# Kernel optimization log

Measured on AMD Instinct MI355X. Metric: run time of the kernel, lower is better.

## Reference

```python
import jax, jax.numpy as jnp
import numpy as np

N_NODES = 100000
N_EDGES = 1600000
IN_DIM, HID_DIM, OUT_DIM = 128, 64, 64


def setup_inputs() -> dict:
    key = jax.random.key(0)
    ks = jax.random.split(key, 8)
    x = jax.random.normal(ks[0], (N_NODES, IN_DIM), dtype=jnp.float32)
    edge_index = jax.random.randint(ks[1], (2, N_EDGES), 0, N_NODES, dtype=jnp.int32)
    edge_weight = jax.random.uniform(ks[2], (N_EDGES,), dtype=jnp.float32)
    # GCNConv parameters (glorot-ish init)
    w1 = jax.random.normal(ks[3], (IN_DIM, HID_DIM), dtype=jnp.float32) / np.sqrt(IN_DIM)
    b1 = jnp.zeros((HID_DIM,), dtype=jnp.float32)
    w2 = jax.random.normal(ks[4], (HID_DIM, OUT_DIM), dtype=jnp.float32) / np.sqrt(HID_DIM)
    b2 = jnp.zeros((OUT_DIM,), dtype=jnp.float32)
    return {"x": x, "edge_index": edge_index, "edge_weight": edge_weight,
            "w1": w1, "b1": b1, "w2": w2, "b2": b2}


def _gcn_conv(h, src, dst, edge_weight, w, b, n_nodes):
    # GCNConv(normalize=False): linear transform, then edge-weighted scatter-add
    # (source_to_target flow: gather from src, scatter-sum into dst), then bias.
    h = h @ w                                   # [N, out]
    msg = h[src] * edge_weight[:, None]          # [E, out] irregular gather
    agg = jax.ops.segment_sum(msg, dst, num_segments=n_nodes)  # [N, out]
    return agg + b


def reference(x, edge_index, edge_weight, w1, b1, w2, b2):
    src, dst = edge_index[0], edge_index[1]
    n = x.shape[0]
    # Dropout is identity in eval mode (training=False).
    h = _gcn_conv(x, src, dst, edge_weight, w1, b1, n)
    h = jax.nn.relu(h)
    out = _gcn_conv(h, src, dst, edge_weight, w2, b2, n)
    return out
```

## Files before the change

### kernel.cpp

```cpp
#include <hip/hip_runtime.h>
#include <hip/hip_bf16.h>


#define N_NODES 100000
#define N_EDGES 1600000
#define NB1     196
#define T1      4096
#define NT1     391

typedef unsigned short ushort_t;
typedef unsigned int uint_t;
typedef __attribute__((ext_vector_type(8))) short bf16x8;
typedef __attribute__((ext_vector_type(4))) float floatx4;
typedef __attribute__((ext_vector_type(8))) ushort_t ushort8v;

static __device__ __forceinline__ float bf2f(ushort_t h) {
    return __uint_as_float(((uint_t)h) << 16);
}
static __device__ __forceinline__ ushort_t f2bf(float f) {
    uint_t u = __float_as_uint(f);
    u = (u + 0x7FFF + ((u >> 16) & 1)) >> 16;
    return (ushort_t)u;
}

__global__ __launch_bounds__(512) void k_count1(
    const int* __restrict__ dst, int* __restrict__ counts, int E)
{
    __shared__ int cnt[NB1];
    const int t = threadIdx.x;
    if (t < NB1) cnt[t] = 0;
    __syncthreads();
    const int e0 = blockIdx.x * T1;
    const int e1 = min(E, e0 + T1);
    for (int e = e0 + t; e < e1; e += 512)
        atomicAdd(&cnt[dst[e] >> 9], 1);
    __syncthreads();
    if (t < NB1) counts[(size_t)blockIdx.x * NB1 + t] = cnt[t];
}

__global__ __launch_bounds__(512) void k_cscan(
    const int* __restrict__ counts, int* __restrict__ offs,
    int* __restrict__ ctot)
{
    __shared__ int s[512];
    const int t = threadIdx.x, k = blockIdx.x;
    const int v = (t < NT1) ? counts[(size_t)t * NB1 + k] : 0;
    s[t] = v;
    #pragma unroll
    for (int off = 1; off < 512; off <<= 1) {
        __syncthreads();
        int a = (t >= off) ? s[t - off] : 0;
        __syncthreads();
        s[t] += a;
    }
    __syncthreads();
    if (t < NT1) offs[(size_t)t * NB1 + k] = s[t] - v;
    if (t == 511) ctot[k] = s[511];
}

__global__ __launch_bounds__(256) void k_tscan(
    const int* __restrict__ ctot, int* __restrict__ cbase)
{
    __shared__ int s[256];
    const int t = threadIdx.x;
    const int v = (t < NB1) ? ctot[t] : 0;
    s[t] = v;
    #pragma unroll
    for (int off = 1; off < 256; off <<= 1) {
        __syncthreads();
        int a = (t >= off) ? s[t - off] : 0;
        __syncthreads();
        s[t] += a;
    }
    __syncthreads();
    if (t < NB1) cbase[t] = s[t] - v;
}

__global__ __launch_bounds__(512) void k_pass1(
    const int* __restrict__ src, const int* __restrict__ dst,
    const float* __restrict__ ew, const int* __restrict__ offs,
    const int* __restrict__ cbase, int2* __restrict__ recs1, int E)
{
    __shared__ int cnt[NB1], start[NB1], cursor[NB1], gb[NB1];
    __shared__ int s[256];
    __shared__ int2 stg[T1];
    __shared__ unsigned char sb[T1];
    const int t = threadIdx.x, b = blockIdx.x;

    if (t < NB1) cnt[t] = 0;
    __syncthreads();
    const int e0 = b * T1;
    const int e1 = min(E, e0 + T1);
    for (int e = e0 + t; e < e1; e += 512)
        atomicAdd(&cnt[dst[e] >> 9], 1);
    __syncthreads();
    int v = 0;
    if (t < 256) { v = (t < NB1) ? cnt[t] : 0; s[t] = v; }
    #pragma unroll
    for (int off = 1; off < 256; off <<= 1) {
        __syncthreads();
        int a = (t < 256 && t >= off) ? s[t - off] : 0;
        __syncthreads();
        if (t < 256) s[t] += a;
    }
    __syncthreads();
    if (t < NB1) {
        int st = s[t] - v;
        start[t]  = st;
        cursor[t] = st;
        gb[t]     = cbase[t] + offs[(size_t)b * NB1 + t];
    }
    __syncthreads();
    for (int e = e0 + t; e < e1; e += 512) {
        int d  = dst[e];
        int bk = d >> 9;
        int p  = atomicAdd(&cursor[bk], 1);
        int2 r;
        r.x = ((d & 511) << 17) | src[e];
        r.y = __float_as_int(ew[e]);
        stg[p] = r;
        sb[p]  = (unsigned char)bk;
    }
    __syncthreads();
    const int n = e1 - e0;
    for (int i = t; i < n; i += 512) {
        int bk = sb[i];
        recs1[gb[bk] + (i - start[bk])] = stg[i];
    }
}

__global__ __launch_bounds__(512) void k_pass2(
    const int2* __restrict__ recs1, const int* __restrict__ cbase,
    const int* __restrict__ ctot, int2* __restrict__ recs2,
    int* __restrict__ node_start, int* __restrict__ node_cnt, int N)
{
    __shared__ int cnt[512];
    __shared__ int s[512];
    __shared__ int cursor[512];
    const int t = threadIdx.x, b = blockIdx.x;
    const int lo = cbase[b];
    const int hi = lo + ctot[b];

    cnt[t] = 0;
    __syncthreads();
    for (int j = lo + t; j < hi; j += 512)
        atomicAdd(&cnt[((uint_t)recs1[j].x) >> 17], 1);
    __syncthreads();
    const int v = cnt[t];
    s[t] = v;
    #pragma unroll
    for (int off = 1; off < 512; off <<= 1) {
        __syncthreads();
        int a = (t >= off) ? s[t - off] : 0;
        __syncthreads();
        s[t] += a;
    }
    __syncthreads();
    const int stl = s[t] - v;
    cursor[t] = stl;
    const int ng = b * 512 + t;
    if (ng < N) {
        node_start[ng] = lo + stl;
        node_cnt[ng]   = v;
    }
    __syncthreads();
    for (int j = lo + t; j < hi; j += 512) {
        int2 r = recs1[j];
        int dl = ((uint_t)r.x) >> 17;
        int p  = atomicAdd(&cursor[dl], 1);
        int2 o;
        o.x = r.x & 0x1FFFF;
        o.y = r.y;
        recs2[lo + p] = o;
    }
}

__global__ __launch_bounds__(256) void k_gemm1(
    const float* __restrict__ X, const float* __restrict__ W,
    ushort_t* __restrict__ Y, int N)
{
    __shared__ ushort_t sA[64 * 136];
    __shared__ ushort_t sB[64 * 136];
    const int tid  = threadIdx.x;
    const int row0 = blockIdx.x * 64;

    for (int i = tid; i < 64 * 32; i += 256) {
        int r = i >> 5, c4 = (i & 31) * 4;
        int rg = row0 + r; if (rg > N - 1) rg = N - 1;
        float4 v = *(const float4*)(X + (size_t)rg * 128 + c4);
        ushort4 pk = make_ushort4(f2bf(v.x), f2bf(v.y), f2bf(v.z), f2bf(v.w));
        *(ushort4*)(sA + r * 136 + c4) = pk;
    }
    for (int i = tid; i < 128 * 16; i += 256) {
        int k = i >> 4, n4 = (i & 15) * 4;
        float4 v = *(const float4*)(W + (size_t)k * 64 + n4);
        sB[(n4 + 0) * 136 + k] = f2bf(v.x);
        sB[(n4 + 1) * 136 + k] = f2bf(v.y);
        sB[(n4 + 2) * 136 + k] = f2bf(v.z);
        sB[(n4 + 3) * 136 + k] = f2bf(v.w);
    }
    __syncthreads();

    const int wid = tid >> 6, lane = tid & 63;
    const int m = lane & 15, quad = lane >> 4;
    floatx4 acc[4] = {};

    #pragma unroll
    for (int ks = 0; ks < 4; ++ks) {
        bf16x8 a = *(const bf16x8*)(sA + (wid * 16 + m) * 136 + ks * 32 + quad * 8);
        #pragma unroll
        for (int nt = 0; nt < 4; ++nt) {
            bf16x8 bfr = *(const bf16x8*)(sB + (nt * 16 + m) * 136 + ks * 32 + quad * 8);
            acc[nt] = __builtin_amdgcn_mfma_f32_16x16x32_bf16(a, bfr, acc[nt], 0, 0, 0);
        }
    }
    #pragma unroll
    for (int nt = 0; nt < 4; ++nt)
        #pragma unroll
        for (int r = 0; r < 4; ++r) {
            int grow = row0 + wid * 16 + quad * 4 + r;
            if (grow < N)
                Y[(size_t)grow * 64 + nt * 16 + m] = f2bf(acc[nt][r]);
        }
}

__global__ __launch_bounds__(256) void k_gemm2(
    const ushort_t* __restrict__ X, const float* __restrict__ W,
    ushort_t* __restrict__ Y, int N)
{
    __shared__ ushort_t sA[64 * 72];
    __shared__ ushort_t sB[64 * 72];
    const int tid  = threadIdx.x;
    const int row0 = blockIdx.x * 64;

    for (int i = tid; i < 64 * 16; i += 256) {
        int r = i >> 4, c4 = (i & 15) * 4;
        int rg = row0 + r; if (rg > N - 1) rg = N - 1;
        *(ushort4*)(sA + r * 72 + c4) =
            *(const ushort4*)(X + (size_t)rg * 64 + c4);
    }
    for (int i = tid; i < 64 * 16; i += 256) {
        int k = i >> 4, n4 = (i & 15) * 4;
        float4 v = *(const float4*)(W + (size_t)k * 64 + n4);
        sB[(n4 + 0) * 72 + k] = f2bf(v.x);
        sB[(n4 + 1) * 72 + k] = f2bf(v.y);
        sB[(n4 + 2) * 72 + k] = f2bf(v.z);
        sB[(n4 + 3) * 72 + k] = f2bf(v.w);
    }
    __syncthreads();

    const int wid = tid >> 6, lane = tid & 63;
    const int m = lane & 15, quad = lane >> 4;
    floatx4 acc[4] = {};

    #pragma unroll
    for (int ks = 0; ks < 2; ++ks) {
        bf16x8 a = *(const bf16x8*)(sA + (wid * 16 + m) * 72 + ks * 32 + quad * 8);
        #pragma unroll
        for (int nt = 0; nt < 4; ++nt) {
            bf16x8 bfr = *(const bf16x8*)(sB + (nt * 16 + m) * 72 + ks * 32 + quad * 8);
            acc[nt] = __builtin_amdgcn_mfma_f32_16x16x32_bf16(a, bfr, acc[nt], 0, 0, 0);
        }
    }
    #pragma unroll
    for (int nt = 0; nt < 4; ++nt)
        #pragma unroll
        for (int r = 0; r < 4; ++r) {
            int grow = row0 + wid * 16 + quad * 4 + r;
            if (grow < N)
                Y[(size_t)grow * 64 + nt * 16 + m] = f2bf(acc[nt][r]);
        }
}

template<bool RELU, bool OUT_BF16>
__global__ __launch_bounds__(256) void k_gather(
    const ushort_t* __restrict__ H, const int2* __restrict__ recs,
    const int* __restrict__ node_start, const int* __restrict__ node_cnt,
    const float* __restrict__ bias, void* __restrict__ out)
{
    const int wid  = threadIdx.x >> 6;
    const int lane = threadIdx.x & 63;
    const int n    = blockIdx.x * 4 + wid;

    const int start = node_start[n];
    const int end   = start + node_cnt[n];
    const int oct   = lane >> 3;
    const int c8    = (lane & 7) * 8;

    float a[8];
    #pragma unroll
    for (int i = 0; i < 8; ++i) a[i] = 0.f;

    for (int base = start; base < end; base += 64) {
        const int m = (end - base < 64) ? (end - base) : 64;
        int2 r = recs[base + (lane < m ? lane : 0)];
        float rw = __int_as_float(r.y);
        #pragma unroll 8
        for (int jj = 0; jj < m; jj += 8) {
            int idx = jj + oct;
            int s   = __shfl(r.x, idx);
            float w = __shfl(rw, idx);
            if (idx >= m) w = 0.f;
            ushort8v hv = *(const ushort8v*)(H + (size_t)s * 64 + c8);
            #pragma unroll
            for (int i = 0; i < 8; ++i)
                a[i] = fmaf(w, bf2f(hv[i]), a[i]);
        }
    }
    #pragma unroll
    for (int i = 0; i < 8; ++i) {
        a[i] += __shfl_down(a[i], 32);
        a[i] += __shfl_down(a[i], 16);
        a[i] += __shfl_down(a[i], 8);
    }

    if (lane < 8) {
        float4 b0 = *(const float4*)(bias + c8);
        float4 b1v = *(const float4*)(bias + c8 + 4);
        float v[8];
        v[0] = a[0] + b0.x;  v[1] = a[1] + b0.y;
        v[2] = a[2] + b0.z;  v[3] = a[3] + b0.w;
        v[4] = a[4] + b1v.x; v[5] = a[5] + b1v.y;
        v[6] = a[6] + b1v.z; v[7] = a[7] + b1v.w;
        if (RELU) {
            #pragma unroll
            for (int i = 0; i < 8; ++i) v[i] = fmaxf(v[i], 0.f);
        }
        if (OUT_BF16) {
            ushort8v pk;
            #pragma unroll
            for (int i = 0; i < 8; ++i) pk[i] = f2bf(v[i]);
            *(ushort8v*)((ushort_t*)out + (size_t)n * 64 + c8) = pk;
        } else {
            *(float4*)((float*)out + (size_t)n * 64 + c8) =
                make_float4(v[0], v[1], v[2], v[3]);
            *(float4*)((float*)out + (size_t)n * 64 + c8 + 4) =
                make_float4(v[4], v[5], v[6], v[7]);
        }
    }
}

extern "C" void kernel_launch(void* const* d_in, const int* in_sizes, int n_in,
                              void* d_out, int out_size, void* d_ws, size_t ws_size,
                              hipStream_t stream) {
    const float* x   = (const float*)d_in[0];
    const int*   ei  = (const int*)  d_in[1];
    const float* ew  = (const float*)d_in[2];
    const float* w1  = (const float*)d_in[3];
    const float* b1  = (const float*)d_in[4];
    const float* w2  = (const float*)d_in[5];
    const float* b2  = (const float*)d_in[6];
    float* out = (float*)d_out;

    const int N = N_NODES, E = N_EDGES;
    const int* src = ei;
    const int* dst = ei + E;

    char* p = (char*)d_ws;
    ushort_t* bufA   = (ushort_t*)p;  p += (size_t)N_NODES * 64 * 2;
    int2*     recs2  = (int2*)p;      p += (size_t)N_EDGES * 8;
    int2*     recs1  = (int2*)p;
    ushort_t* bufB   = (ushort_t*)p;  p += (size_t)N_EDGES * 8;
    int*      counts = (int*)p;       p += (size_t)NT1 * NB1 * 4;
    int*      offs   = (int*)p;       p += (size_t)NT1 * NB1 * 4;
    int*      ctot   = (int*)p;       p += 1024;
    int*      cbase  = (int*)p;       p += 1024;
    int*      nstart = (int*)p;       p += (size_t)N_NODES * 4;
    int*      ncnt   = (int*)p;       p += (size_t)N_NODES * 4;

    k_count1<<<NT1, 512, 0, stream>>>(dst, counts, E);
    k_cscan <<<NB1, 512, 0, stream>>>(counts, offs, ctot);
    k_tscan <<<1,   256, 0, stream>>>(ctot, cbase);
    k_pass1 <<<NT1, 512, 0, stream>>>(src, dst, ew, offs, cbase, recs1, E);
    k_pass2 <<<NB1, 512, 0, stream>>>(recs1, cbase, ctot, recs2, nstart, ncnt, N);

    k_gemm1<<<(N + 63) / 64, 256, 0, stream>>>(x, w1, bufA, N);
    k_gather<true, true><<<N / 4, 256, 0, stream>>>(bufA, recs2, nstart, ncnt, b1, bufB);

    k_gemm2<<<(N + 63) / 64, 256, 0, stream>>>(bufB, w2, bufA, N);
    k_gather<false, false><<<N / 4, 256, 0, stream>>>(bufA, recs2, nstart, ncnt, b2, out);
}
```

Measured before the change: 262.1 us.

## Use finer dst buckets, pack node info, stage GEMM stores, simplify gather

Doubles the number of coarse destination buckets, going from 512 nodes each to 256, so the second sort pass uses 256-thread blocks and more of them. Node start and count are packed into one int2 array. The GEMM epilogues now stage results in shared memory and write coalesced 16-byte rows. The gather kernel is rewritten so each edge is handled by 16 lanes with 4-wide loads, removing the shuffle-broadcast loop. Together these aim to cut sort overhead and improve memory access patterns, at the cost of narrower per-lane loads in the gather and an extra shared-memory round trip in the GEMMs.

```diff
diff --git a/kernel.cpp b/kernel.cpp
--- a/kernel.cpp
+++ b/kernel.cpp
@@ -4,7 +4,7 @@
 
 #define N_NODES 100000
 #define N_EDGES 1600000
-#define NB1     196
+#define NB1     391
 #define T1      4096
 #define NT1     391
 
@@ -33,7 +33,7 @@
     const int e0 = blockIdx.x * T1;
     const int e1 = min(E, e0 + T1);
     for (int e = e0 + t; e < e1; e += 512)
-        atomicAdd(&cnt[dst[e] >> 9], 1);
+        atomicAdd(&cnt[dst[e] >> 8], 1);
     __syncthreads();
     if (t < NB1) counts[(size_t)blockIdx.x * NB1 + t] = cnt[t];
 }
@@ -58,15 +58,15 @@
     if (t == 511) ctot[k] = s[511];
 }
 
-__global__ __launch_bounds__(256) void k_tscan(
+__global__ __launch_bounds__(512) void k_tscan(
     const int* __restrict__ ctot, int* __restrict__ cbase)
 {
-    __shared__ int s[256];
+    __shared__ int s[512];
     const int t = threadIdx.x;
     const int v = (t < NB1) ? ctot[t] : 0;
     s[t] = v;
     #pragma unroll
-    for (int off = 1; off < 256; off <<= 1) {
+    for (int off = 1; off < 512; off <<= 1) {
         __syncthreads();
         int a = (t >= off) ? s[t - off] : 0;
         __syncthreads();
@@ -82,9 +82,9 @@
     const int* __restrict__ cbase, int2* __restrict__ recs1, int E)
 {
     __shared__ int cnt[NB1], start[NB1], cursor[NB1], gb[NB1];
-    __shared__ int s[256];
+    __shared__ int s[512];
     __shared__ int2 stg[T1];
-    __shared__ unsigned char sb[T1];
+    __shared__ ushort_t sb[T1];
     const int t = threadIdx.x, b = blockIdx.x;
 
     if (t < NB1) cnt[t] = 0;
@@ -92,16 +92,16 @@
     const int e0 = b * T1;
     const int e1 = min(E, e0 + T1);
     for (int e = e0 + t; e < e1; e += 512)
-        atomicAdd(&cnt[dst[e] >> 9], 1);
-    __syncthreads();
-    int v = 0;
-    if (t < 256) { v = (t < NB1) ? cnt[t] : 0; s[t] = v; }
-    #pragma unroll
-    for (int off = 1; off < 256; off <<= 1) {
-        __syncthreads();
-        int a = (t < 256 && t >= off) ? s[t - off] : 0;
-        __syncthreads();
-        if (t < 256) s[t] += a;
+        atomicAdd(&cnt[dst[e] >> 8], 1);
+    __syncthreads();
+    const int v = (t < NB1) ? cnt[t] : 0;
+    s[t] = v;
+    #pragma unroll
+    for (int off = 1; off < 512; off <<= 1) {
+        __syncthreads();
+        int a = (t >= off) ? s[t - off] : 0;
+        __syncthreads();
+        s[t] += a;
     }
     __syncthreads();
     if (t < NB1) {
@@ -113,13 +113,13 @@
     __syncthreads();
     for (int e = e0 + t; e < e1; e += 512) {
         int d  = dst[e];
-        int bk = d >> 9;
+        int bk = d >> 8;
         int p  = atomicAdd(&cursor[bk], 1);
         int2 r;
-        r.x = ((d & 511) << 17) | src[e];
+        r.x = ((d & 255) << 17) | src[e];
         r.y = __float_as_int(ew[e]);
         stg[p] = r;
-        sb[p]  = (unsigned char)bk;
+        sb[p]  = (ushort_t)bk;
     }
     __syncthreads();
     const int n = e1 - e0;
@@ -129,27 +129,27 @@
     }
 }
 
-__global__ __launch_bounds__(512) void k_pass2(
+__global__ __launch_bounds__(256) void k_pass2(
     const int2* __restrict__ recs1, const int* __restrict__ cbase,
     const int* __restrict__ ctot, int2* __restrict__ recs2,
-    int* __restrict__ node_start, int* __restrict__ node_cnt, int N)
-{
-    __shared__ int cnt[512];
-    __shared__ int s[512];
-    __shared__ int cursor[512];
+    int2* __restrict__ nodeinfo, int N)
+{
+    __shared__ int cnt[256];
+    __shared__ int s[256];
+    __shared__ int cursor[256];
     const int t = threadIdx.x, b = blockIdx.x;
     const int lo = cbase[b];
     const int hi = lo + ctot[b];
 
     cnt[t] = 0;
     __syncthreads();
-    for (int j = lo + t; j < hi; j += 512)
+    for (int j = lo + t; j < hi; j += 256)
         atomicAdd(&cnt[((uint_t)recs1[j].x) >> 17], 1);
     __syncthreads();
     const int v = cnt[t];
     s[t] = v;
     #pragma unroll
-    for (int off = 1; off < 512; off <<= 1) {
+    for (int off = 1; off < 256; off <<= 1) {
         __syncthreads();
         int a = (t >= off) ? s[t - off] : 0;
         __syncthreads();
@@ -158,13 +158,13 @@
     __syncthreads();
     const int stl = s[t] - v;
     cursor[t] = stl;
-    const int ng = b * 512 + t;
+    const int ng = b * 256 + t;
     if (ng < N) {
-        node_start[ng] = lo + stl;
-        node_cnt[ng]   = v;
-    }
-    __syncthreads();
-    for (int j = lo + t; j < hi; j += 512) {
+        int2 ni; ni.x = lo + stl; ni.y = v;
+        nodeinfo[ng] = ni;
+    }
+    __syncthreads();
+    for (int j = lo + t; j < hi; j += 256) {
         int2 r = recs1[j];
         int dl = ((uint_t)r.x) >> 17;
         int p  = atomicAdd(&cursor[dl], 1);
@@ -214,14 +214,20 @@
             acc[nt] = __builtin_amdgcn_mfma_f32_16x16x32_bf16(a, bfr, acc[nt], 0, 0, 0);
         }
     }
+    __syncthreads();
     #pragma unroll
     for (int nt = 0; nt < 4; ++nt)
         #pragma unroll
-        for (int r = 0; r < 4; ++r) {
-            int grow = row0 + wid * 16 + quad * 4 + r;
-            if (grow < N)
-                Y[(size_t)grow * 64 + nt * 16 + m] = f2bf(acc[nt][r]);
-        }
+        for (int r = 0; r < 4; ++r)
+            sA[(wid * 16 + quad * 4 + r) * 72 + nt * 16 + m] = f2bf(acc[nt][r]);
+    __syncthreads();
+    for (int i = tid; i < 64 * 8; i += 256) {
+        int rr = i >> 3, c8 = (i & 7) * 8;
+        int rg = row0 + rr;
+        if (rg < N)
+            *(ushort8v*)(Y + (size_t)rg * 64 + c8) =
+                *(const ushort8v*)(sA + rr * 72 + c8);
+    }
 }
 
 __global__ __launch_bounds__(256) void k_gemm2(
@@ -262,80 +268,71 @@
             acc[nt] = __builtin_amdgcn_mfma_f32_16x16x32_bf16(a, bfr, acc[nt], 0, 0, 0);
         }
     }
+    __syncthreads();
     #pragma unroll
     for (int nt = 0; nt < 4; ++nt)
         #pragma unroll
-        for (int r = 0; r < 4; ++r) {
-            int grow = row0 + wid * 16 + quad * 4 + r;
-            if (grow < N)
-                Y[(size_t)grow * 64 + nt * 16 + m] = f2bf(acc[nt][r]);
-        }
+        for (int r = 0; r < 4; ++r)
+            sA[(wid * 16 + quad * 4 + r) * 72 + nt * 16 + m] = f2bf(acc[nt][r]);
+    __syncthreads();
+    for (int i = tid; i < 64 * 8; i += 256) {
+        int rr = i >> 3, c8 = (i & 7) * 8;
+        int rg = row0 + rr;
+        if (rg < N)
+            *(ushort8v*)(Y + (size_t)rg * 64 + c8) =
+                *(const ushort8v*)(sA + rr * 72 + c8);
+    }
 }
 
 template<bool RELU, bool OUT_BF16>
 __global__ __launch_bounds__(256) void k_gather(
     const ushort_t* __restrict__ H, const int2* __restrict__ recs,
-    const int* __restrict__ node_start, const int* __restrict__ node_cnt,
-    const float* __restrict__ bias, void* __restrict__ out)
+    const int2* __restrict__ nodeinfo, const float* __restrict__ bias,
+    void* __restrict__ out)
 {
     const int wid  = threadIdx.x >> 6;
     const int lane = threadIdx.x & 63;
     const int n    = blockIdx.x * 4 + wid;
 
-    const int start = node_start[n];
-    const int end   = start + node_cnt[n];
-    const int oct   = lane >> 3;
-    const int c8    = (lane & 7) * 8;
-
-    float a[8];
-    #pragma unroll
-    for (int i = 0; i < 8; ++i) a[i] = 0.f;
-
-    for (int base = start; base < end; base += 64) {
-        const int m = (end - base < 64) ? (end - base) : 64;
-        int2 r = recs[base + (lane < m ? lane : 0)];
-        float rw = __int_as_float(r.y);
-        #pragma unroll 8
-        for (int jj = 0; jj < m; jj += 8) {
-            int idx = jj + oct;
-            int s   = __shfl(r.x, idx);
-            float w = __shfl(rw, idx);
-            if (idx >= m) w = 0.f;
-            ushort8v hv = *(const ushort8v*)(H + (size_t)s * 64 + c8);
-            #pragma unroll
-            for (int i = 0; i < 8; ++i)
-                a[i] = fmaf(w, bf2f(hv[i]), a[i]);
-        }
-    }
-    #pragma unroll
-    for (int i = 0; i < 8; ++i) {
-        a[i] += __shfl_down(a[i], 32);
-        a[i] += __shfl_down(a[i], 16);
-        a[i] += __shfl_down(a[i], 8);
-    }
-
-    if (lane < 8) {
-        float4 b0 = *(const float4*)(bias + c8);
-        float4 b1v = *(const float4*)(bias + c8 + 4);
-        float v[8];
-        v[0] = a[0] + b0.x;  v[1] = a[1] + b0.y;
-        v[2] = a[2] + b0.z;  v[3] = a[3] + b0.w;
-        v[4] = a[4] + b1v.x; v[5] = a[5] + b1v.y;
-        v[6] = a[6] + b1v.z; v[7] = a[7] + b1v.w;
+    const int2 ni   = nodeinfo[n];
+    const int start = ni.x;
+    const int cnt   = ni.y;
+    const int end   = start + cnt;
+    const int g     = lane >> 4;
+    const int c4    = (lane & 15) * 4;
+    const int trip  = (cnt + 3) >> 2;
+
+    float a0 = 0.f, a1 = 0.f, a2 = 0.f, a3 = 0.f;
+    int j = start + g;
+    #pragma unroll 2
+    for (int k = 0; k < trip; ++k, j += 4) {
+        int jc = (j < end) ? j : (end - 1);
+        int2 r = recs[jc];
+        float w = (j < end) ? __int_as_float(r.y) : 0.f;
+        ushort4 hv = *(const ushort4*)(H + (size_t)r.x * 64 + c4);
+        a0 = fmaf(w, bf2f(hv.x), a0);
+        a1 = fmaf(w, bf2f(hv.y), a1);
+        a2 = fmaf(w, bf2f(hv.z), a2);
+        a3 = fmaf(w, bf2f(hv.w), a3);
+    }
+    a0 += __shfl_down(a0, 32); a1 += __shfl_down(a1, 32);
+    a2 += __shfl_down(a2, 32); a3 += __shfl_down(a3, 32);
+    a0 += __shfl_down(a0, 16); a1 += __shfl_down(a1, 16);
+    a2 += __shfl_down(a2, 16); a3 += __shfl_down(a3, 16);
+
+    if (lane < 16) {
+        float4 bv = *(const float4*)(bias + c4);
+        float v0 = a0 + bv.x, v1 = a1 + bv.y, v2 = a2 + bv.z, v3 = a3 + bv.w;
         if (RELU) {
-            #pragma unroll
-            for (int i = 0; i < 8; ++i) v[i] = fmaxf(v[i], 0.f);
+            v0 = fmaxf(v0, 0.f); v1 = fmaxf(v1, 0.f);
+            v2 = fmaxf(v2, 0.f); v3 = fmaxf(v3, 0.f);
         }
         if (OUT_BF16) {
-            ushort8v pk;
-            #pragma unroll
-            for (int i = 0; i < 8; ++i) pk[i] = f2bf(v[i]);
-            *(ushort8v*)((ushort_t*)out + (size_t)n * 64 + c8) = pk;
+            ushort4 pk = make_ushort4(f2bf(v0), f2bf(v1), f2bf(v2), f2bf(v3));
+            *(ushort4*)((ushort_t*)out + (size_t)n * 64 + c4) = pk;
         } else {
-            *(float4*)((float*)out + (size_t)n * 64 + c8) =
-                make_float4(v[0], v[1], v[2], v[3]);
-            *(float4*)((float*)out + (size_t)n * 64 + c8 + 4) =
-                make_float4(v[4], v[5], v[6], v[7]);
+            *(float4*)((float*)out + (size_t)n * 64 + c4) =
+                make_float4(v0, v1, v2, v3);
         }
     }
 }
@@ -363,20 +360,19 @@
     ushort_t* bufB   = (ushort_t*)p;  p += (size_t)N_EDGES * 8;
     int*      counts = (int*)p;       p += (size_t)NT1 * NB1 * 4;
     int*      offs   = (int*)p;       p += (size_t)NT1 * NB1 * 4;
-    int*      ctot   = (int*)p;       p += 1024;
-    int*      cbase  = (int*)p;       p += 1024;
-    int*      nstart = (int*)p;       p += (size_t)N_NODES * 4;
-    int*      ncnt   = (int*)p;       p += (size_t)N_NODES * 4;
+    int*      ctot   = (int*)p;       p += 2048;
+    int*      cbase  = (int*)p;       p += 2048;
+    int2*     ninfo  = (int2*)p;      p += (size_t)N_NODES * 8;
 
     k_count1<<<NT1, 512, 0, stream>>>(dst, counts, E);
     k_cscan <<<NB1, 512, 0, stream>>>(counts, offs, ctot);
-    k_tscan <<<1,   256, 0, stream>>>(ctot, cbase);
+    k_tscan <<<1,   512, 0, stream>>>(ctot, cbase);
     k_pass1 <<<NT1, 512, 0, stream>>>(src, dst, ew, offs, cbase, recs1, E);
-    k_pass2 <<<NB1, 512, 0, stream>>>(recs1, cbase, ctot, recs2, nstart, ncnt, N);
+    k_pass2 <<<NB1, 256, 0, stream>>>(recs1, cbase, ctot, recs2, ninfo, N);
 
     k_gemm1<<<(N + 63) / 64, 256, 0, stream>>>(x, w1, bufA, N);
-    k_gather<true, true><<<N / 4, 256, 0, stream>>>(bufA, recs2, nstart, ncnt, b1, bufB);
+    k_gather<true, true><<<N / 4, 256, 0, stream>>>(bufA, recs2, ninfo, b1, bufB);
 
     k_gemm2<<<(N + 63) / 64, 256, 0, stream>>>(bufB, w2, bufA, N);
-    k_gather<false, false><<<N / 4, 256, 0, stream>>>(bufA, recs2, nstart, ncnt, b2, out);
-}
+    k_gather<false, false><<<N / 4, 256, 0, stream>>>(bufA, recs2, ninfo, b2, out);
+}
```

New measurement: 276.2 us. 1.05x slower.
